# Optimization experiments

Measured on AMD Instinct MI355X. Metric: run time of the kernel, lower is better.

The kernel has to match this reference:

```python
import jax, jax.numpy as jnp
import numpy as np

VOCAB = 32000
EMB = 512
STATE = 512
B = 4
S = 1024


def setup_inputs() -> dict:
    key = jax.random.key(0)
    ks = jax.random.split(key, 6)
    x = jax.random.randint(ks[0], (B, S), 0, VOCAB)
    emb_table = jax.random.normal(ks[1], (VOCAB, EMB), dtype=jnp.float32)
    a = jax.random.normal(ks[2], (STATE, STATE), dtype=jnp.float32) * 0.02
    b = jax.random.normal(ks[3], (EMB, STATE), dtype=jnp.float32) * 0.02
    # nn.Linear(state, vocab): weight [vocab, state], bias [vocab]
    lim = 1.0 / np.sqrt(STATE)
    c_w = jax.random.uniform(ks[4], (VOCAB, STATE), minval=-lim, maxval=lim, dtype=jnp.float32)
    c_b = jax.random.uniform(ks[5], (VOCAB,), minval=-lim, maxval=lim, dtype=jnp.float32)
    return {"x": x, "emb_table": emb_table, "a": a, "b": b, "c_w": c_w, "c_b": c_b}


def reference(x, emb_table, a, b, c_w, c_b):
    emb = emb_table[x]                      # [B, S, E]
    # Precompute input projection for all timesteps (single GEMM).
    u = jnp.einsum('bse,en->bsn', emb, b)   # [B, S, N]
    u_t = jnp.swapaxes(u, 0, 1)             # [S, B, N] for scan

    def step(state, u_step):
        new_state = jnp.tanh(state @ a + u_step)  # [B, N]
        return new_state, new_state

    init = jnp.zeros((x.shape[0], a.shape[0]), dtype=emb.dtype)
    _, states = jax.lax.scan(step, init, u_t)   # states: [S, B, N]
    # Readout (dropout=0 -> identity). One big GEMM over all timesteps.
    logits = jnp.einsum('sbn,vn->sbv', states, c_w) + c_b  # [S, B, V]
    return jnp.swapaxes(logits, 0, 1)           # [B, S, V]
```

## Files before the change

### kernel.cpp

```cpp
#include <hip/hip_runtime.h>
#include <hip/hip_fp16.h>

typedef _Float16 f16;
typedef _Float16 f16x8 __attribute__((ext_vector_type(8)));
typedef _Float16 f16x4 __attribute__((ext_vector_type(4)));
typedef float f32x4v __attribute__((ext_vector_type(4)));
typedef unsigned long long u64;

#define S_LEN 1024
#define NS 512
#define NV 32000
#define NW 4
#define SENT 0x7C007C007C007C00ULL
#define FUSED_LDS 98304

#define MFMA16(a, b, c) __builtin_amdgcn_mfma_f32_16x16x32_f16((a), (b), (c), 0, 0, 0)


__global__ __launch_bounds__(256) void transpose512_f16_kernel(
        const float* __restrict__ src, f16* __restrict__ dstT,
        u64* __restrict__ X) {
    int idx = blockIdx.x * 256 + threadIdx.x;
    X[idx] = SENT;
    X[idx + 262144] = SENT;
    int r = idx >> 9;
    int c = idx & 511;
    dstT[c * 512 + r] = (f16)src[idx];
}

__global__ __launch_bounds__(256) void embu_kernel(
        const int* __restrict__ x, const float* __restrict__ emb,
        const f16* __restrict__ bT, f16* __restrict__ u16) {
    __shared__ f16 embA[64 * 40];
    __shared__ f16 Bt[512 * 40];
    __shared__ int xi[64];

    int t = threadIdx.x;
    int wg = blockIdx.x;
    if (t < 64) {
        int m = wg * 64 + t;
        int bb = m & 3, ss = m >> 2;
        xi[t] = x[bb * S_LEN + ss];
    }
    __syncthreads();

    int wv = t >> 6, l = t & 63, lr = l & 15, lg = l >> 4;

    f32x4v acc[32];
#pragma unroll
    for (int i = 0; i < 32; i++) acc[i] = (f32x4v){0.f, 0.f, 0.f, 0.f};

    for (int kc = 0; kc < 512; kc += 32) {
        __syncthreads();
        {
            int tk = t >> 2, c0 = (t & 3) * 8;
            const float* src = emb + (size_t)xi[tk] * NS + kc + c0;
            float4 v0 = *(const float4*)src;
            float4 v1 = *(const float4*)(src + 4);
            f16x8 h;
            h[0] = (f16)v0.x; h[1] = (f16)v0.y; h[2] = (f16)v0.z; h[3] = (f16)v0.w;
            h[4] = (f16)v1.x; h[5] = (f16)v1.y; h[6] = (f16)v1.z; h[7] = (f16)v1.w;
            *(f16x8*)&embA[tk * 40 + c0] = h;
        }
        {
            int c0 = (t & 3) * 8;
            int n0 = t >> 2;
#pragma unroll
            for (int rr = 0; rr < 8; rr++) {
                int n = rr * 64 + n0;
                f16x8 v = *(const f16x8*)&bT[n * 512 + kc + c0];
                *(f16x8*)&Bt[n * 40 + c0] = v;
            }
        }
        __syncthreads();

        f16x8 af = *(const f16x8*)&embA[(wv * 16 + lr) * 40 + 8 * lg];
#pragma unroll
        for (int vt = 0; vt < 32; vt++) {
            f16x8 bf = *(const f16x8*)&Bt[(vt * 16 + lr) * 40 + 8 * lg];
            acc[vt] = MFMA16(af, bf, acc[vt]);
        }
    }

    int m0 = wg * 64 + wv * 16 + 4 * lg;
    int ss = m0 >> 2;
#pragma unroll
    for (int vt = 0; vt < 32; vt++) {
        int n = vt * 16 + lr;
        f16x4 h;
#pragma unroll
        for (int i = 0; i < 4; i++) h[i] = (f16)acc[vt][i];
        *(f16x4*)&u16[((size_t)ss * NS + n) * 4] = h;
    }
}

__global__ __launch_bounds__(512) void fused_kernel(
        const float* __restrict__ a, const f16* __restrict__ u16,
        const float* __restrict__ cw, const float* __restrict__ cb,
        u64* __restrict__ X, float* __restrict__ out) {
    extern __shared__ char smem[];
    int t = threadIdx.x;
    int bid = blockIdx.x;
    int w = t >> 6, l = t & 63, lr = l & 15, lg = l >> 4;

    if (bid < NW) {
        f16* Sb = (f16*)smem;
        int r = bid;
        int col = r * 128 + w * 16 + lr;

        int gcol = -1;
        if (w < 6) {
            int cwk = w + (w >= 2 * r ? 2 : 0);
            gcol = cwk * 64 + l;
        }

        for (int i = t; i < 2 * 4 * 544; i += 512) Sb[i] = (f16)0.f;

        f16x8 afr[16];
#pragma unroll
        for (int ks = 0; ks < 16; ks++) {
            f16x8 h;
#pragma unroll
            for (int j = 0; j < 8; j++)
                h[j] = (f16)a[(size_t)(ks * 32 + 8 * lg + j) * NS + col];
            afr[ks] = h;
        }

        f16x4 upf = *(const f16x4*)&u16[(size_t)col * 4];

        __syncthreads();

#pragma unroll 1
        for (int s = 0; s < S_LEN; s++) {
            int cur = s & 1, nxt = cur ^ 1;

            f32x4v acca, accb;
            acca[0] = (float)upf[0]; acca[1] = (float)upf[1];
            acca[2] = (float)upf[2]; acca[3] = (float)upf[3];
            accb = (f32x4v){0.f, 0.f, 0.f, 0.f};

            {
                int sn = (s + 1 < S_LEN) ? s + 1 : S_LEN - 1;
                upf = *(const f16x4*)&u16[((size_t)sn * NS + col) * 4];
            }

            const char* sb = (const char*)Sb + cur * 4352 +
                             (lr & 3) * 1088 + lg * 16;
#pragma unroll
            for (int ks = 0; ks < 16; ks += 2) {
                f16x8 s0 = *(const f16x8*)(sb + ks * 64);
                f16x8 s1 = *(const f16x8*)(sb + ks * 64 + 64);
                acca = MFMA16(s0, afr[ks], acca);
                accb = MFMA16(s1, afr[ks + 1], accb);
            }

            if (lg == 0) {
                union { u64 u; f16 h[4]; } pk;
#pragma unroll
                for (int i = 0; i < 4; i++) {
                    float y = acca[i] + accb[i];
                    float e = __expf(2.0f * y);
                    float rc = __builtin_amdgcn_rcpf(e + 1.0f);
                    y = __builtin_fmaf(-2.0f, rc, 1.0f);
                    pk.h[i] = (f16)y;
                }
                __hip_atomic_store(&X[(size_t)s * NS + col], pk.u,
                                   __ATOMIC_RELAXED, __HIP_MEMORY_SCOPE_AGENT);
#pragma unroll
                for (int i = 0; i < 4; i++)
                    Sb[nxt * 2176 + i * 544 + col] = pk.h[i];
            }

            if (s == S_LEN - 1) break;

            if (w < 6) {
                u64 v;
                do {
                    v = __hip_atomic_load(&X[(size_t)s * NS + gcol],
                                          __ATOMIC_RELAXED,
                                          __HIP_MEMORY_SCOPE_AGENT);
                } while (v == SENT);
                union { u64 u; f16 h[4]; } pk;
                pk.u = v;
#pragma unroll
                for (int i = 0; i < 4; i++)
                    Sb[nxt * 2176 + i * 544 + gcol] = pk.h[i];
            }

            asm volatile("s_waitcnt lgkmcnt(0)" ::: "memory");
            __builtin_amdgcn_s_barrier();
            __builtin_amdgcn_sched_barrier(0);
        }
        return;
    }

    f16* Ast = (f16*)smem;
    f16* Bw = (f16*)(smem + 256 * 72 * 2);

    int idx = bid - NW;
    int bm = idx / 250;
    int bn = idx % 250;
    int s0 = bm * 64;

    if (t == 0) {
        int sc = (bm == 15) ? (S_LEN - 1) : (s0 + 64);
        while (__hip_atomic_load(&X[(size_t)sc * NS], __ATOMIC_RELAXED,
                                 __HIP_MEMORY_SCOPE_AGENT) == SENT)
            __builtin_amdgcn_s_sleep(16);
    }
    __syncthreads();

    int wr = w >> 1, wc = w & 1;

    f32x4v acc[4][4];
#pragma unroll
    for (int i = 0; i < 4; i++)
#pragma unroll
        for (int j = 0; j < 4; j++) acc[i][j] = (f32x4v){0.f, 0.f, 0.f, 0.f};

    for (int kc = 0; kc < 512; kc += 64) {
        __syncthreads();
        {
            int srel = t >> 3;
            int ck = (t & 7) * 8;
            const u64* xs = &X[(size_t)(s0 + srel) * NS + kc + ck];
            u64 v[8];
#pragma unroll
            for (int j = 0; j < 8; j++)
                v[j] = __hip_atomic_load(&xs[j], __ATOMIC_RELAXED,
                                         __HIP_MEMORY_SCOPE_AGENT);
#pragma unroll
            for (int j = 0; j < 8; j++)
                while (v[j] == SENT)
                    v[j] = __hip_atomic_load(&xs[j], __ATOMIC_RELAXED,
                                             __HIP_MEMORY_SCOPE_AGENT);
#pragma unroll
            for (int j = 0; j < 8; j++) {
                union { u64 u; f16 h[4]; } pk;
                pk.u = v[j];
#pragma unroll
                for (int b = 0; b < 4; b++)
                    Ast[(srel * 4 + b) * 72 + ck + j] = pk.h[b];
            }
        }
#pragma unroll
        for (int q = 0; q < 4; q++) {
            int i2 = q * 512 + t;
            int row = i2 >> 4;
            int c0 = (i2 & 15) * 4;
            float4 v = *(const float4*)&cw[(size_t)(bn * 128 + row) * NS + kc + c0];
            f16x4 h;
            h[0] = (f16)v.x; h[1] = (f16)v.y; h[2] = (f16)v.z; h[3] = (f16)v.w;
            *(f16x4*)&Bw[row * 72 + c0] = h;
        }
        __syncthreads();

#pragma unroll
        for (int ks = 0; ks < 2; ks++) {
            f16x8 af[4], bf[4];
#pragma unroll
            for (int mt = 0; mt < 4; mt++)
                af[mt] = *(const f16x8*)&Ast[(wr * 64 + mt * 16 + lr) * 72 +
                                             ks * 32 + 8 * lg];
#pragma unroll
            for (int vt = 0; vt < 4; vt++)
                bf[vt] = *(const f16x8*)&Bw[(wc * 64 + vt * 16 + lr) * 72 +
                                            ks * 32 + 8 * lg];
#pragma unroll
            for (int mt = 0; mt < 4; mt++)
#pragma unroll
                for (int vt = 0; vt < 4; vt++)
                    acc[mt][vt] = MFMA16(af[mt], bf[vt], acc[mt][vt]);
        }
    }

    float bias[4];
#pragma unroll
    for (int vt = 0; vt < 4; vt++)
        bias[vt] = cb[bn * 128 + wc * 64 + vt * 16 + lr];

#pragma unroll
    for (int mt = 0; mt < 4; mt++) {
#pragma unroll
        for (int i = 0; i < 4; i++) {
            int m = bm * 256 + wr * 64 + mt * 16 + 4 * lg + i;
            int bb = m & 3, ss = m >> 2;
            float* orow = out + (size_t)(bb * S_LEN + ss) * NV + bn * 128 + wc * 64;
#pragma unroll
            for (int vt = 0; vt < 4; vt++)
                orow[vt * 16 + lr] = acc[mt][vt][i] + bias[vt];
        }
    }
}

extern "C" void kernel_launch(void* const* d_in, const int* in_sizes, int n_in,
                              void* d_out, int out_size, void* d_ws, size_t ws_size,
                              hipStream_t stream) {
    (void)in_sizes; (void)n_in; (void)out_size; (void)ws_size;

    const int*   x   = (const int*)d_in[0];
    const float* emb = (const float*)d_in[1];
    const float* a   = (const float*)d_in[2];
    const float* bm  = (const float*)d_in[3];
    const float* cw  = (const float*)d_in[4];
    const float* cb  = (const float*)d_in[5];
    float* out = (float*)d_out;

    char* ws = (char*)d_ws;
    f16* u16 = (f16*)(ws);
    u64* X   = (u64*)(ws + (4u << 20));
    f16* bT16 = (f16*)(ws + (8u << 20));

    hipFuncSetAttribute(reinterpret_cast<const void*>(fused_kernel),
                        hipFuncAttributeMaxDynamicSharedMemorySize,
                        FUSED_LDS);

    transpose512_f16_kernel<<<1024, 256, 0, stream>>>(bm, bT16, X);
    embu_kernel<<<64, 256, 0, stream>>>(x, emb, bT16, u16);
    fused_kernel<<<NW + 16 * 250, 512, FUSED_LDS, stream>>>(
        a, u16, cw, cb, X, out);
}
```

Measured before the change: 1.351 ms.

## Split recurrence over 8 blocks with dedicated compute and gather warps

The sequential tanh recurrence now runs across 8 workgroups instead of 4, so each one owns 64 state columns. Within a workgroup, four warps do the MFMA matvec and four warps only poll global memory for other blocks' columns and copy them into LDS. This halves per-block MFMA work per step and moves the polling off the compute warps. In exchange, each step waits on more cross-block exchanges, and the GEMM part of the kernel gets four fewer blocks.

Measured after the change: 1.422 ms. 1.05x slower.

```diff
diff --git a/kernel.cpp b/kernel.cpp
--- a/kernel.cpp
+++ b/kernel.cpp
@@ -10,7 +10,7 @@
 #define S_LEN 1024
 #define NS 512
 #define NV 32000
-#define NW 4
+#define NW 8
 #define SENT 0x7C007C007C007C00ULL
 #define FUSED_LDS 98304
 
@@ -106,90 +106,115 @@
     if (bid < NW) {
         f16* Sb = (f16*)smem;
         int r = bid;
-        int col = r * 128 + w * 16 + lr;
-
-        int gcol = -1;
-        if (w < 6) {
-            int cwk = w + (w >= 2 * r ? 2 : 0);
-            gcol = cwk * 64 + l;
-        }
 
         for (int i = t; i < 2 * 4 * 544; i += 512) Sb[i] = (f16)0.f;
 
-        f16x8 afr[16];
-#pragma unroll
-        for (int ks = 0; ks < 16; ks++) {
-            f16x8 h;
-#pragma unroll
-            for (int j = 0; j < 8; j++)
-                h[j] = (f16)a[(size_t)(ks * 32 + 8 * lg + j) * NS + col];
-            afr[ks] = h;
-        }
-
-        f16x4 upf = *(const f16x4*)&u16[(size_t)col * 4];
-
-        __syncthreads();
+        if (w < 4) {
+            int col = r * 64 + w * 16 + lr;
+
+            f16x8 afr[16];
+#pragma unroll
+            for (int ks = 0; ks < 16; ks++) {
+                f16x8 h;
+#pragma unroll
+                for (int j = 0; j < 8; j++)
+                    h[j] = (f16)a[(size_t)(ks * 32 + 8 * lg + j) * NS + col];
+                afr[ks] = h;
+            }
+
+            f16x4 upf = *(const f16x4*)&u16[(size_t)col * 4];
+
+            __syncthreads();
 
 #pragma unroll 1
-        for (int s = 0; s < S_LEN; s++) {
-            int cur = s & 1, nxt = cur ^ 1;
-
-            f32x4v acca, accb;
-            acca[0] = (float)upf[0]; acca[1] = (float)upf[1];
-            acca[2] = (float)upf[2]; acca[3] = (float)upf[3];
-            accb = (f32x4v){0.f, 0.f, 0.f, 0.f};
-
-            {
-                int sn = (s + 1 < S_LEN) ? s + 1 : S_LEN - 1;
-                upf = *(const f16x4*)&u16[((size_t)sn * NS + col) * 4];
-            }
-
-            const char* sb = (const char*)Sb + cur * 4352 +
-                             (lr & 3) * 1088 + lg * 16;
-#pragma unroll
-            for (int ks = 0; ks < 16; ks += 2) {
-                f16x8 s0 = *(const f16x8*)(sb + ks * 64);
-                f16x8 s1 = *(const f16x8*)(sb + ks * 64 + 64);
-                acca = MFMA16(s0, afr[ks], acca);
-                accb = MFMA16(s1, afr[ks + 1], accb);
-            }
-
-            if (lg == 0) {
+            for (int s = 0; s < S_LEN; s++) {
+                int cur = s & 1, nxt = cur ^ 1;
+
+                f32x4v acca, accb;
+                acca[0] = (float)upf[0]; acca[1] = (float)upf[1];
+                acca[2] = (float)upf[2]; acca[3] = (float)upf[3];
+                accb = (f32x4v){0.f, 0.f, 0.f, 0.f};
+
+                {
+                    int sn = (s + 1 < S_LEN) ? s + 1 : S_LEN - 1;
+                    upf = *(const f16x4*)&u16[((size_t)sn * NS + col) * 4];
+                }
+
+                const char* sb = (const char*)Sb + cur * 4352 +
+                                 (lr & 3) * 1088 + lg * 16;
+#pragma unroll
+                for (int ks = 0; ks < 16; ks += 2) {
+                    f16x8 s0 = *(const f16x8*)(sb + ks * 64);
+                    f16x8 s1 = *(const f16x8*)(sb + ks * 64 + 64);
+                    acca = MFMA16(s0, afr[ks], acca);
+                    accb = MFMA16(s1, afr[ks + 1], accb);
+                }
+
+                if (lg == 0) {
+                    union { u64 u; f16 h[4]; } pk;
+#pragma unroll
+                    for (int i = 0; i < 4; i++) {
+                        float y = acca[i] + accb[i];
+                        float e = __expf(2.0f * y);
+                        float rc = __builtin_amdgcn_rcpf(e + 1.0f);
+                        y = __builtin_fmaf(-2.0f, rc, 1.0f);
+                        pk.h[i] = (f16)y;
+                    }
+                    __hip_atomic_store(&X[(size_t)s * NS + col], pk.u,
+                                       __ATOMIC_RELAXED,
+                                       __HIP_MEMORY_SCOPE_AGENT);
+#pragma unroll
+                    for (int i = 0; i < 4; i++)
+                        Sb[nxt * 2176 + i * 544 + col] = pk.h[i];
+                }
+
+                if (s == S_LEN - 1) break;
+
+                asm volatile("s_waitcnt lgkmcnt(0)" ::: "memory");
+                __builtin_amdgcn_s_barrier();
+                __builtin_amdgcn_sched_barrier(0);
+            }
+        } else {
+            int i0 = (w - 4) * 64 + l;
+            int col0 = (i0 < r * 64) ? i0 : i0 + 64;
+            int i1 = i0 + 256;
+            int col1 = (i1 < 448) ? ((i1 < r * 64) ? i1 : i1 + 64) : -1;
+
+            __syncthreads();
+
+#pragma unroll 1
+            for (int s = 0; s < S_LEN - 1; s++) {
+                int nxt = (s & 1) ^ 1;
+
+                u64 v0 = SENT;
+                u64 v1 = (col1 >= 0) ? SENT : 0ULL;
+                const u64* p0 = &X[(size_t)s * NS + col0];
+                const u64* p1 = &X[(size_t)s * NS + (col1 >= 0 ? col1 : 0)];
+                while (v0 == SENT || v1 == SENT) {
+                    if (v0 == SENT)
+                        v0 = __hip_atomic_load(p0, __ATOMIC_RELAXED,
+                                               __HIP_MEMORY_SCOPE_AGENT);
+                    if (v1 == SENT)
+                        v1 = __hip_atomic_load(p1, __ATOMIC_RELAXED,
+                                               __HIP_MEMORY_SCOPE_AGENT);
+                }
+
                 union { u64 u; f16 h[4]; } pk;
-#pragma unroll
-                for (int i = 0; i < 4; i++) {
-                    float y = acca[i] + accb[i];
-                    float e = __expf(2.0f * y);
-                    float rc = __builtin_amdgcn_rcpf(e + 1.0f);
-                    y = __builtin_fmaf(-2.0f, rc, 1.0f);
-                    pk.h[i] = (f16)y;
-                }
-                __hip_atomic_store(&X[(size_t)s * NS + col], pk.u,
-                                   __ATOMIC_RELAXED, __HIP_MEMORY_SCOPE_AGENT);
+                pk.u = v0;
 #pragma unroll
                 for (int i = 0; i < 4; i++)
-                    Sb[nxt * 2176 + i * 544 + col] = pk.h[i];
-            }
-
-            if (s == S_LEN - 1) break;
-
-            if (w < 6) {
-                u64 v;
-                do {
-                    v = __hip_atomic_load(&X[(size_t)s * NS + gcol],
-                                          __ATOMIC_RELAXED,
-                                          __HIP_MEMORY_SCOPE_AGENT);
-                } while (v == SENT);
-                union { u64 u; f16 h[4]; } pk;
-                pk.u = v;
-#pragma unroll
-                for (int i = 0; i < 4; i++)
-                    Sb[nxt * 2176 + i * 544 + gcol] = pk.h[i];
-            }
-
-            asm volatile("s_waitcnt lgkmcnt(0)" ::: "memory");
-            __builtin_amdgcn_s_barrier();
-            __builtin_amdgcn_sched_barrier(0);
+                    Sb[nxt * 2176 + i * 544 + col0] = pk.h[i];
+                if (col1 >= 0) {
+                    pk.u = v1;
+#pragma unroll
+                    for (int i = 0; i < 4; i++)
+                        Sb[nxt * 2176 + i * 544 + col1] = pk.h[i];
+                }
+
+                asm volatile("s_waitcnt lgkmcnt(0)" ::: "memory");
+                __builtin_amdgcn_s_barrier();
+                __builtin_amdgcn_sched_barrier(0);
+            }
         }
         return;
     }
```

## Replace per-step workgroup barrier with LDS flag sync and dedicated fetcher waves

Applied to the files above, without the earlier changes.

The recurrence blocks grow to 12 waves. Eight compute waves use per-wave LDS progress flags instead of a full barrier each step. Four new fetcher waves poll remote state columns from global memory into a triple-buffered LDS slot, so compute waves can start on locally produced k-chunks before remote data arrives. GEMM blocks are launched with 768 threads but only the first 512 do work, which may hurt occupancy of the readout GEMM.

After: 1.641 ms. 21.5% more time.

```diff
diff --git a/kernel.cpp b/kernel.cpp
--- a/kernel.cpp
+++ b/kernel.cpp
@@ -13,6 +13,7 @@
 #define NW 4
 #define SENT 0x7C007C007C007C00ULL
 #define FUSED_LDS 98304
+#define TPB 768
 
 #define MFMA16(a, b, c) __builtin_amdgcn_mfma_f32_16x16x32_f16((a), (b), (c), 0, 0, 0)
 
@@ -94,7 +95,7 @@
     }
 }
 
-__global__ __launch_bounds__(512) void fused_kernel(
+__global__ __launch_bounds__(TPB) void fused_kernel(
         const float* __restrict__ a, const f16* __restrict__ u16,
         const float* __restrict__ cw, const float* __restrict__ cb,
         u64* __restrict__ X, float* __restrict__ out) {
@@ -105,91 +106,154 @@
 
     if (bid < NW) {
         f16* Sb = (f16*)smem;
+        int* flg = (int*)(smem + 3 * 4 * 544 * 2);
         int r = bid;
-        int col = r * 128 + w * 16 + lr;
-
-        int gcol = -1;
-        if (w < 6) {
-            int cwk = w + (w >= 2 * r ? 2 : 0);
-            gcol = cwk * 64 + l;
-        }
-
-        for (int i = t; i < 2 * 4 * 544; i += 512) Sb[i] = (f16)0.f;
-
-        f16x8 afr[16];
-#pragma unroll
-        for (int ks = 0; ks < 16; ks++) {
-            f16x8 h;
-#pragma unroll
-            for (int j = 0; j < 8; j++)
-                h[j] = (f16)a[(size_t)(ks * 32 + 8 * lg + j) * NS + col];
-            afr[ks] = h;
-        }
-
-        f16x4 upf = *(const f16x4*)&u16[(size_t)col * 4];
-
-        __syncthreads();
+
+        for (int i = t; i < 3 * 4 * 544; i += TPB) Sb[i] = (f16)0.f;
+        if (t < 16) flg[t] = 0;
+        __syncthreads();
+
+        if (w < 8) {
+            int col = r * 128 + w * 16 + lr;
+
+            f16x8 afr_own[4], afr_rem[12];
+#pragma unroll
+            for (int q = 0; q < 4; q++) {
+                int k = 4 * r + q;
+                f16x8 h;
+#pragma unroll
+                for (int j = 0; j < 8; j++)
+                    h[j] = (f16)a[(size_t)(k * 32 + 8 * lg + j) * NS + col];
+                afr_own[q] = h;
+            }
+#pragma unroll
+            for (int idx = 0; idx < 12; idx++) {
+                int k = idx + (idx >= 4 * r ? 4 : 0);
+                f16x8 h;
+#pragma unroll
+                for (int j = 0; j < 8; j++)
+                    h[j] = (f16)a[(size_t)(k * 32 + 8 * lg + j) * NS + col];
+                afr_rem[idx] = h;
+            }
+
+            f16x4 upf = *(const f16x4*)&u16[(size_t)col * 4];
+            int cs = 0;
 
 #pragma unroll 1
-        for (int s = 0; s < S_LEN; s++) {
-            int cur = s & 1, nxt = cur ^ 1;
-
-            f32x4v acca, accb;
-            acca[0] = (float)upf[0]; acca[1] = (float)upf[1];
-            acca[2] = (float)upf[2]; acca[3] = (float)upf[3];
-            accb = (f32x4v){0.f, 0.f, 0.f, 0.f};
-
-            {
-                int sn = (s + 1 < S_LEN) ? s + 1 : S_LEN - 1;
-                upf = *(const f16x4*)&u16[((size_t)sn * NS + col) * 4];
-            }
-
-            const char* sb = (const char*)Sb + cur * 4352 +
-                             (lr & 3) * 1088 + lg * 16;
-#pragma unroll
-            for (int ks = 0; ks < 16; ks += 2) {
-                f16x8 s0 = *(const f16x8*)(sb + ks * 64);
-                f16x8 s1 = *(const f16x8*)(sb + ks * 64 + 64);
-                acca = MFMA16(s0, afr[ks], acca);
-                accb = MFMA16(s1, afr[ks + 1], accb);
-            }
-
-            if (lg == 0) {
+            for (int s = 0; s < S_LEN; s++) {
+                int ns = (cs == 2) ? 0 : cs + 1;
+
+                f32x4v acc;
+                acc[0] = (float)upf[0]; acc[1] = (float)upf[1];
+                acc[2] = (float)upf[2]; acc[3] = (float)upf[3];
+                {
+                    int sn = (s + 1 < S_LEN) ? s + 1 : S_LEN - 1;
+                    upf = *(const f16x4*)&u16[((size_t)sn * NS + col) * 4];
+                }
+
+                const char* sbc = (const char*)Sb + cs * 4352 +
+                                  (lr & 3) * 1088 + lg * 16;
+
+#pragma unroll
+                for (int q = 0; q < 4; q++) {
+                    int k = 4 * r + q;
+                    if (l == 0) {
+                        while (__hip_atomic_load(&flg[2 * q], __ATOMIC_RELAXED,
+                                   __HIP_MEMORY_SCOPE_WORKGROUP) < s ||
+                               __hip_atomic_load(&flg[2 * q + 1], __ATOMIC_RELAXED,
+                                   __HIP_MEMORY_SCOPE_WORKGROUP) < s) {}
+                    }
+                    __builtin_amdgcn_sched_barrier(0);
+                    f16x8 sf = *(const f16x8*)(sbc + k * 64);
+                    acc = MFMA16(sf, afr_own[q], acc);
+                }
+#pragma unroll
+                for (int g = 0; g < 4; g++) {
+                    if (l == 0) {
+                        while (__hip_atomic_load(&flg[8 + g], __ATOMIC_RELAXED,
+                                   __HIP_MEMORY_SCOPE_WORKGROUP) < s) {}
+                    }
+                    __builtin_amdgcn_sched_barrier(0);
+#pragma unroll
+                    for (int i = 0; i < 3; i++) {
+                        int idx = g * 3 + i;
+                        int k = idx + (idx >= 4 * r ? 4 : 0);
+                        f16x8 sf = *(const f16x8*)(sbc + k * 64);
+                        acc = MFMA16(sf, afr_rem[idx], acc);
+                    }
+                }
+
                 union { u64 u; f16 h[4]; } pk;
-#pragma unroll
-                for (int i = 0; i < 4; i++) {
-                    float y = acca[i] + accb[i];
-                    float e = __expf(2.0f * y);
-                    float rc = __builtin_amdgcn_rcpf(e + 1.0f);
-                    y = __builtin_fmaf(-2.0f, rc, 1.0f);
-                    pk.h[i] = (f16)y;
-                }
-                __hip_atomic_store(&X[(size_t)s * NS + col], pk.u,
-                                   __ATOMIC_RELAXED, __HIP_MEMORY_SCOPE_AGENT);
-#pragma unroll
-                for (int i = 0; i < 4; i++)
-                    Sb[nxt * 2176 + i * 544 + col] = pk.h[i];
-            }
-
-            if (s == S_LEN - 1) break;
-
-            if (w < 6) {
-                u64 v;
-                do {
-                    v = __hip_atomic_load(&X[(size_t)s * NS + gcol],
-                                          __ATOMIC_RELAXED,
-                                          __HIP_MEMORY_SCOPE_AGENT);
-                } while (v == SENT);
-                union { u64 u; f16 h[4]; } pk;
-                pk.u = v;
-#pragma unroll
-                for (int i = 0; i < 4; i++)
-                    Sb[nxt * 2176 + i * 544 + gcol] = pk.h[i];
-            }
-
-            asm volatile("s_waitcnt lgkmcnt(0)" ::: "memory");
-            __builtin_amdgcn_s_barrier();
-            __builtin_amdgcn_sched_barrier(0);
+                if (lg == 0) {
+#pragma unroll
+                    for (int i = 0; i < 4; i++) {
+                        float y = acc[i];
+                        float e = __expf(2.0f * y);
+                        float rc = __builtin_amdgcn_rcpf(e + 1.0f);
+                        y = __builtin_fmaf(-2.0f, rc, 1.0f);
+                        pk.h[i] = (f16)y;
+                    }
+                    __hip_atomic_store(&X[(size_t)s * NS + col], pk.u,
+                                       __ATOMIC_RELAXED, __HIP_MEMORY_SCOPE_AGENT);
+                }
+                if (s == S_LEN - 1) break;
+
+                if (lg == 0) {
+                    f16* sbn = Sb + ns * 2176;
+#pragma unroll
+                    for (int i = 0; i < 4; i++)
+                        sbn[i * 544 + col] = pk.h[i];
+                }
+                asm volatile("s_waitcnt lgkmcnt(0)" ::: "memory");
+                __builtin_amdgcn_sched_barrier(0);
+                if (l == 0)
+                    __hip_atomic_store(&flg[w], s + 1, __ATOMIC_RELAXED,
+                                       __HIP_MEMORY_SCOPE_WORKGROUP);
+                cs = ns;
+            }
+        } else {
+            int gw = w - 8;
+            int i0 = gw * 3 + (l >> 5);
+            int k0 = i0 + (i0 >= 4 * r ? 4 : 0);
+            int colA = k0 * 32 + (l & 31);
+            int i2 = gw * 3 + 2;
+            int k2 = i2 + (i2 >= 4 * r ? 4 : 0);
+            int colB = (l < 32) ? (k2 * 32 + l) : colA;
+
+            int nb = 1;
+#pragma unroll 1
+            for (int g = 0; g < S_LEN - 1; g++) {
+                const u64* pA = &X[(size_t)g * NS + colA];
+                const u64* pB = &X[(size_t)g * NS + colB];
+                u64 vA = SENT;
+                u64 vB = (l < 32) ? SENT : 0ULL;
+                while (vA == SENT || vB == SENT) {
+                    if (vA == SENT)
+                        vA = __hip_atomic_load(pA, __ATOMIC_RELAXED,
+                                               __HIP_MEMORY_SCOPE_AGENT);
+                    if (vB == SENT)
+                        vB = __hip_atomic_load(pB, __ATOMIC_RELAXED,
+                                               __HIP_MEMORY_SCOPE_AGENT);
+                }
+                __builtin_amdgcn_sched_barrier(0);
+                f16* sbn = Sb + nb * 2176;
+                union { u64 u; f16 h[4]; } pa;
+                pa.u = vA;
+#pragma unroll
+                for (int i = 0; i < 4; i++) sbn[i * 544 + colA] = pa.h[i];
+                if (l < 32) {
+                    union { u64 u; f16 h[4]; } pb;
+                    pb.u = vB;
+#pragma unroll
+                    for (int i = 0; i < 4; i++) sbn[i * 544 + colB] = pb.h[i];
+                }
+                asm volatile("s_waitcnt lgkmcnt(0)" ::: "memory");
+                __builtin_amdgcn_sched_barrier(0);
+                if (l == 0)
+                    __hip_atomic_store(&flg[8 + gw], g + 1, __ATOMIC_RELAXED,
+                                       __HIP_MEMORY_SCOPE_WORKGROUP);
+                nb = (nb == 2) ? 0 : nb + 1;
+            }
         }
         return;
     }
@@ -220,75 +284,82 @@
 
     for (int kc = 0; kc < 512; kc += 64) {
         __syncthreads();
-        {
-            int srel = t >> 3;
-            int ck = (t & 7) * 8;
-            const u64* xs = &X[(size_t)(s0 + srel) * NS + kc + ck];
-            u64 v[8];
-#pragma unroll
-            for (int j = 0; j < 8; j++)
-                v[j] = __hip_atomic_load(&xs[j], __ATOMIC_RELAXED,
-                                         __HIP_MEMORY_SCOPE_AGENT);
-#pragma unroll
-            for (int j = 0; j < 8; j++)
-                while (v[j] == SENT)
+        if (t < 512) {
+            {
+                int srel = t >> 3;
+                int ck = (t & 7) * 8;
+                const u64* xs = &X[(size_t)(s0 + srel) * NS + kc + ck];
+                u64 v[8];
+#pragma unroll
+                for (int j = 0; j < 8; j++)
                     v[j] = __hip_atomic_load(&xs[j], __ATOMIC_RELAXED,
                                              __HIP_MEMORY_SCOPE_AGENT);
 #pragma unroll
-            for (int j = 0; j < 8; j++) {
-                union { u64 u; f16 h[4]; } pk;
-                pk.u = v[j];
-#pragma unroll
-                for (int b = 0; b < 4; b++)
-                    Ast[(srel * 4 + b) * 72 + ck + j] = pk.h[b];
-            }
-        }
-#pragma unroll
-        for (int q = 0; q < 4; q++) {
-            int i2 = q * 512 + t;
-            int row = i2 >> 4;
-            int c0 = (i2 & 15) * 4;
-            float4 v = *(const float4*)&cw[(size_t)(bn * 128 + row) * NS + kc + c0];
-            f16x4 h;
-            h[0] = (f16)v.x; h[1] = (f16)v.y; h[2] = (f16)v.z; h[3] = (f16)v.w;
-            *(f16x4*)&Bw[row * 72 + c0] = h;
-        }
-        __syncthreads();
-
-#pragma unroll
-        for (int ks = 0; ks < 2; ks++) {
-            f16x8 af[4], bf[4];
-#pragma unroll
-            for (int mt = 0; mt < 4; mt++)
-                af[mt] = *(const f16x8*)&Ast[(wr * 64 + mt * 16 + lr) * 72 +
-                                             ks * 32 + 8 * lg];
-#pragma unroll
-            for (int vt = 0; vt < 4; vt++)
-                bf[vt] = *(const f16x8*)&Bw[(wc * 64 + vt * 16 + lr) * 72 +
-                                            ks * 32 + 8 * lg];
-#pragma unroll
-            for (int mt = 0; mt < 4; mt++)
+                for (int j = 0; j < 8; j++)
+                    while (v[j] == SENT)
+                        v[j] = __hip_atomic_load(&xs[j], __ATOMIC_RELAXED,
+                                                 __HIP_MEMORY_SCOPE_AGENT);
+#pragma unroll
+                for (int j = 0; j < 8; j++) {
+                    union { u64 u; f16 h[4]; } pk;
+                    pk.u = v[j];
+#pragma unroll
+                    for (int b = 0; b < 4; b++)
+                        Ast[(srel * 4 + b) * 72 + ck + j] = pk.h[b];
+                }
+            }
+#pragma unroll
+            for (int q = 0; q < 4; q++) {
+                int i2 = q * 512 + t;
+                int row = i2 >> 4;
+                int c0 = (i2 & 15) * 4;
+                float4 v = *(const float4*)&cw[(size_t)(bn * 128 + row) * NS + kc + c0];
+                f16x4 h;
+                h[0] = (f16)v.x; h[1] = (f16)v.y; h[2] = (f16)v.z; h[3] = (f16)v.w;
+                *(f16x4*)&Bw[row * 72 + c0] = h;
+            }
+        }
+        __syncthreads();
+
+        if (w < 8) {
+#pragma unroll
+            for (int ks = 0; ks < 2; ks++) {
+                f16x8 af[4], bf[4];
+#pragma unroll
+                for (int mt = 0; mt < 4; mt++)
+                    af[mt] = *(const f16x8*)&Ast[(wr * 64 + mt * 16 + lr) * 72 +
+                                                 ks * 32 + 8 * lg];
 #pragma unroll
                 for (int vt = 0; vt < 4; vt++)
-                    acc[mt][vt] = MFMA16(af[mt], bf[vt], acc[mt][vt]);
-        }
-    }
-
-    float bias[4];
-#pragma unroll
-    for (int vt = 0; vt < 4; vt++)
-        bias[vt] = cb[bn * 128 + wc * 64 + vt * 16 + lr];
-
-#pragma unroll
-    for (int mt = 0; mt < 4; mt++) {
-#pragma unroll
-        for (int i = 0; i < 4; i++) {
-            int m = bm * 256 + wr * 64 + mt * 16 + 4 * lg + i;
-            int bb = m & 3, ss = m >> 2;
-            float* orow = out + (size_t)(bb * S_LEN + ss) * NV + bn * 128 + wc * 64;
-#pragma unroll
-            for (int vt = 0; vt < 4; vt++)
-                orow[vt * 16 + lr] = acc[mt][vt][i] + bias[vt];
+                    bf[vt] = *(const f16x8*)&Bw[(wc * 64 + vt * 16 + lr) * 72 +
+                                                ks * 32 + 8 * lg];
+#pragma unroll
+                for (int mt = 0; mt < 4; mt++)
+#pragma unroll
+                    for (int vt = 0; vt < 4; vt++)
+                        acc[mt][vt] = MFMA16(af[mt], bf[vt], acc[mt][vt]);
+            }
+        }
+    }
+
+    if (w < 8) {
+        float bias[4];
+#pragma unroll
+        for (int vt = 0; vt < 4; vt++)
+            bias[vt] = cb[bn * 128 + wc * 64 + vt * 16 + lr];
+
+#pragma unroll
+        for (int mt = 0; mt < 4; mt++) {
+#pragma unroll
+            for (int i = 0; i < 4; i++) {
+                int m = bm * 256 + wr * 64 + mt * 16 + 4 * lg + i;
+                int bb = m & 3, ss = m >> 2;
+                float* orow = out + (size_t)(bb * S_LEN + ss) * NV +
+                              bn * 128 + wc * 64;
+#pragma unroll
+                for (int vt = 0; vt < 4; vt++)
+                    orow[vt * 16 + lr] = acc[mt][vt][i] + bias[vt];
+            }
         }
     }
 }
@@ -317,6 +388,6 @@
 
     transpose512_f16_kernel<<<1024, 256, 0, stream>>>(bm, bT16, X);
     embu_kernel<<<64, 256, 0, stream>>>(x, emb, bT16, u16);
-    fused_kernel<<<NW + 16 * 250, 512, FUSED_LDS, stream>>>(
+    fused_kernel<<<NW + 16 * 250, TPB, FUSED_LDS, stream>>>(
         a, u16, cw, cb, X, out);
 }
```
